# Kernel tuning notes

Measured on AMD Instinct MI355X. Metric: run time of the kernel, lower is better.

Reference implementation:

```python
import jax, jax.numpy as jnp
import numpy as np
from jax import lax

KX = np.array([[-1.0, 0.0, 1.0], [-2.0, 0.0, 2.0], [-1.0, 0.0, 1.0]], dtype=np.float32)
KY = np.array([[-1.0, -2.0, -1.0], [0.0, 0.0, 0.0], [1.0, 2.0, 1.0]], dtype=np.float32)


def setup_inputs() -> dict:
    key = jax.random.key(0)
    x = jax.random.normal(key, (16, 64, 256, 256), dtype=jnp.float32)
    return {"x": x}


def _depthwise3x3(x, k2d):
    # x: [B, C, H, W]; k2d: [3, 3] constant Sobel kernel, replicated per channel
    C = x.shape[1]
    w = jnp.broadcast_to(jnp.asarray(k2d, x.dtype), (C, 1, 3, 3))  # OIHW, groups=C
    return lax.conv_general_dilated(
        x, w, window_strides=(1, 1), padding=((1, 1), (1, 1)),
        feature_group_count=C,
        dimension_numbers=("NCHW", "OIHW", "NCHW"))


def reference(x) -> jnp.ndarray:
    edge_x = _depthwise3x3(x, KX)
    edge_y = _depthwise3x3(x, KY)
    edge = jnp.sqrt(edge_x * edge_x + edge_y * edge_y + 1e-12)
    return jnp.mean(edge, axis=1, keepdims=True)  # [B, 1, H, W]
```

## Files before the change

### kernel.cpp

```cpp
#include <hip/hip_runtime.h>
#include <math.h>

#define B_  16
#define C_  64
#define H_  256
#define W_  256
#define R_  8
#define CPW 16

__global__ __launch_bounds__(256) void sobel_kernel(const float* __restrict__ x,
                                                    float* __restrict__ out) {
    const int lane  = threadIdx.x & 63;
    const int wv    = threadIdx.x >> 6;
    const int strip = blockIdx.x;
    const int b     = blockIdx.y;
    const int w0    = lane * 4;
    const int r0    = strip * R_;

    float4 acc[R_];
#pragma unroll
    for (int r = 0; r < R_; ++r) acc[r] = make_float4(0.f, 0.f, 0.f, 0.f);

    const float* xb = x + ((size_t)b * C_ + wv * CPW) * (H_ * W_);

    for (int cc = 0; cc < CPW; ++cc) {
        const float* plane = xb + (size_t)cc * (H_ * W_);

        float4 v[R_ + 2];
#pragma unroll
        for (int rr = 0; rr < R_ + 2; ++rr) {
            int gr  = r0 - 1 + rr;
            int grc = min(max(gr, 0), H_ - 1);
            v[rr] = *(const float4*)(plane + (size_t)grc * W_ + w0);
        }
        if (r0 == 0)        v[0]      = make_float4(0.f, 0.f, 0.f, 0.f);
        if (r0 + R_ == H_)  v[R_ + 1] = make_float4(0.f, 0.f, 0.f, 0.f);

        float4 s0 = make_float4(0,0,0,0), s1 = s0, d0 = s0, d1 = s0;
#pragma unroll
        for (int rr = 0; rr < R_ + 2; ++rr) {
            float4 vr = v[rr];
            float L = __shfl_up(vr.w, 1);
            float R = __shfl_down(vr.x, 1);
            if (lane == 0)  L = 0.f;
            if (lane == 63) R = 0.f;

            float4 s2, d2;
            s2.x = L    + 2.f*vr.x + vr.y;
            s2.y = vr.x + 2.f*vr.y + vr.z;
            s2.z = vr.y + 2.f*vr.z + vr.w;
            s2.w = vr.z + 2.f*vr.w + R;
            d2.x = vr.y - L;
            d2.y = vr.z - vr.x;
            d2.z = vr.w - vr.y;
            d2.w = R    - vr.z;

            if (rr >= 2) {
                float ex, ey;
                ex = d0.x + 2.f*d1.x + d2.x;  ey = s2.x - s0.x;
                acc[rr-2].x += sqrtf(ex*ex + ey*ey + 1e-12f);
                ex = d0.y + 2.f*d1.y + d2.y;  ey = s2.y - s0.y;
                acc[rr-2].y += sqrtf(ex*ex + ey*ey + 1e-12f);
                ex = d0.z + 2.f*d1.z + d2.z;  ey = s2.z - s0.z;
                acc[rr-2].z += sqrtf(ex*ex + ey*ey + 1e-12f);
                ex = d0.w + 2.f*d1.w + d2.w;  ey = s2.w - s0.w;
                acc[rr-2].w += sqrtf(ex*ex + ey*ey + 1e-12f);
            }
            s0 = s1; s1 = s2;
            d0 = d1; d1 = d2;
        }
    }

    __shared__ float part[4][R_][W_];
#pragma unroll
    for (int r = 0; r < R_; ++r)
        *(float4*)&part[wv][r][w0] = acc[r];
    __syncthreads();

    const float scale = 1.f / (float)C_;
    float4* out4 = (float4*)out;
    for (int i = threadIdx.x; i < R_ * (W_ / 4); i += 256) {
        const int row = i >> 6;
        const int c4  = i & 63;
        const float4 p0 = *(const float4*)&part[0][row][c4 * 4];
        const float4 p1 = *(const float4*)&part[1][row][c4 * 4];
        const float4 p2 = *(const float4*)&part[2][row][c4 * 4];
        const float4 p3 = *(const float4*)&part[3][row][c4 * 4];
        float4 s;
        s.x = (((p0.x + p1.x) + p2.x) + p3.x) * scale;
        s.y = (((p0.y + p1.y) + p2.y) + p3.y) * scale;
        s.z = (((p0.z + p1.z) + p2.z) + p3.z) * scale;
        s.w = (((p0.w + p1.w) + p2.w) + p3.w) * scale;
        out4[((size_t)b * H_ + r0 + row) * (W_ / 4) + c4] = s;
    }
}

extern "C" void kernel_launch(void* const* d_in, const int* in_sizes, int n_in,
                              void* d_out, int out_size, void* d_ws, size_t ws_size,
                              hipStream_t stream) {
    const float* x = (const float*)d_in[0];
    float* out = (float*)d_out;
    dim3 grid(H_ / R_, B_);
    sobel_kernel<<<grid, 256, 0, stream>>>(x, out);
}
```

Before: 368.0 us.

## Use 16-row strips, 8 waves per block, XCD-aware block remap and tree reduction

Doubles the row strip height to cut halo reloads, and doubles the block to 8 waves with 8 channels each. Block IDs are remapped so that strips of the same batch land on the same XCD, which should improve L2 reuse of halo rows. The shared-memory reduction becomes a tree across waves, which adds barriers. Only 256 blocks are launched, and the doubled accumulators raise register pressure, which may hurt occupancy.

```diff
diff --git a/kernel.cpp b/kernel.cpp
--- a/kernel.cpp
+++ b/kernel.cpp
@@ -5,23 +5,31 @@
 #define C_  64
 #define H_  256
 #define W_  256
-#define R_  8
-#define CPW 16
+#define R_  16
+#define NW  8
+#define CPW (C_/NW)
 
-__global__ __launch_bounds__(256) void sobel_kernel(const float* __restrict__ x,
-                                                    float* __restrict__ out) {
-    const int lane  = threadIdx.x & 63;
-    const int wv    = threadIdx.x >> 6;
-    const int strip = blockIdx.x;
-    const int b     = blockIdx.y;
-    const int w0    = lane * 4;
-    const int r0    = strip * R_;
+__global__ __launch_bounds__(512, 2) void sobel_kernel(const float* __restrict__ x,
+                                                       float* __restrict__ out) {
+    const int lane = threadIdx.x & 63;
+    const int wv   = threadIdx.x >> 6;
+
+    const int L   = blockIdx.y * gridDim.x + blockIdx.x;
+    const int xcd = L & 7;
+    const int idx = L >> 3;
+    const int P   = xcd * 16 + (idx >> 1);
+    const int sub = idx & 1;
+    const int b     = P >> 3;
+    const int strip = ((P & 7) << 1) | sub;
+
+    const int w0 = lane * 4;
+    const int r0 = strip * R_;
 
     float4 acc[R_];
 #pragma unroll
     for (int r = 0; r < R_; ++r) acc[r] = make_float4(0.f, 0.f, 0.f, 0.f);
 
-    const float* xb = x + ((size_t)b * C_ + wv * CPW) * (H_ * W_);
+    const float* xb = x + ((size_t)b * C_ + wv * CPW) * (size_t)(H_ * W_);
 
     for (int cc = 0; cc < CPW; ++cc) {
         const float* plane = xb + (size_t)cc * (H_ * W_);
@@ -40,20 +48,20 @@
 #pragma unroll
         for (int rr = 0; rr < R_ + 2; ++rr) {
             float4 vr = v[rr];
-            float L = __shfl_up(vr.w, 1);
-            float R = __shfl_down(vr.x, 1);
-            if (lane == 0)  L = 0.f;
-            if (lane == 63) R = 0.f;
+            float Lh = __shfl_up(vr.w, 1);
+            float Rh = __shfl_down(vr.x, 1);
+            if (lane == 0)  Lh = 0.f;
+            if (lane == 63) Rh = 0.f;
 
             float4 s2, d2;
-            s2.x = L    + 2.f*vr.x + vr.y;
+            s2.x = Lh   + 2.f*vr.x + vr.y;
             s2.y = vr.x + 2.f*vr.y + vr.z;
             s2.z = vr.y + 2.f*vr.z + vr.w;
-            s2.w = vr.z + 2.f*vr.w + R;
-            d2.x = vr.y - L;
+            s2.w = vr.z + 2.f*vr.w + Rh;
+            d2.x = vr.y - Lh;
             d2.y = vr.z - vr.x;
             d2.z = vr.w - vr.y;
-            d2.w = R    - vr.z;
+            d2.w = Rh   - vr.z;
 
             if (rr >= 2) {
                 float ex, ey;
@@ -71,27 +79,55 @@
         }
     }
 
-    __shared__ float part[4][R_][W_];
+    __shared__ float part[NW / 2][R_][W_];
+
+    if (wv >= 4) {
 #pragma unroll
-    for (int r = 0; r < R_; ++r)
-        *(float4*)&part[wv][r][w0] = acc[r];
+        for (int r = 0; r < R_; ++r)
+            *(float4*)&part[wv - 4][r][w0] = acc[r];
+    }
     __syncthreads();
-
-    const float scale = 1.f / (float)C_;
-    float4* out4 = (float4*)out;
-    for (int i = threadIdx.x; i < R_ * (W_ / 4); i += 256) {
-        const int row = i >> 6;
-        const int c4  = i & 63;
-        const float4 p0 = *(const float4*)&part[0][row][c4 * 4];
-        const float4 p1 = *(const float4*)&part[1][row][c4 * 4];
-        const float4 p2 = *(const float4*)&part[2][row][c4 * 4];
-        const float4 p3 = *(const float4*)&part[3][row][c4 * 4];
-        float4 s;
-        s.x = (((p0.x + p1.x) + p2.x) + p3.x) * scale;
-        s.y = (((p0.y + p1.y) + p2.y) + p3.y) * scale;
-        s.z = (((p0.z + p1.z) + p2.z) + p3.z) * scale;
-        s.w = (((p0.w + p1.w) + p2.w) + p3.w) * scale;
-        out4[((size_t)b * H_ + r0 + row) * (W_ / 4) + c4] = s;
+    if (wv < 4) {
+#pragma unroll
+        for (int r = 0; r < R_; ++r) {
+            float4 p = *(const float4*)&part[wv][r][w0];
+            acc[r].x += p.x; acc[r].y += p.y; acc[r].z += p.z; acc[r].w += p.w;
+        }
+    }
+    __syncthreads();
+    if (wv == 2 || wv == 3) {
+#pragma unroll
+        for (int r = 0; r < R_; ++r)
+            *(float4*)&part[wv - 2][r][w0] = acc[r];
+    }
+    __syncthreads();
+    if (wv < 2) {
+#pragma unroll
+        for (int r = 0; r < R_; ++r) {
+            float4 p = *(const float4*)&part[wv][r][w0];
+            acc[r].x += p.x; acc[r].y += p.y; acc[r].z += p.z; acc[r].w += p.w;
+        }
+    }
+    __syncthreads();
+    if (wv == 1) {
+#pragma unroll
+        for (int r = 0; r < R_; ++r)
+            *(float4*)&part[0][r][w0] = acc[r];
+    }
+    __syncthreads();
+    if (wv == 0) {
+        const float scale = 1.f / (float)C_;
+        float* ob = out + ((size_t)b * H_ + r0) * W_ + w0;
+#pragma unroll
+        for (int r = 0; r < R_; ++r) {
+            float4 p = *(const float4*)&part[0][r][w0];
+            float4 o;
+            o.x = (acc[r].x + p.x) * scale;
+            o.y = (acc[r].y + p.y) * scale;
+            o.z = (acc[r].z + p.z) * scale;
+            o.w = (acc[r].w + p.w) * scale;
+            *(float4*)(ob + (size_t)r * W_) = o;
+        }
     }
 }
 
@@ -101,5 +137,5 @@
     const float* x = (const float*)d_in[0];
     float* out = (float*)d_out;
     dim3 grid(H_ / R_, B_);
-    sobel_kernel<<<grid, 256, 0, stream>>>(x, out);
+    sobel_kernel<<<grid, 512, 0, stream>>>(x, out);
 }
```

Measured after the change: 395.6 us. +7.5%, slower.
